# Kernel tuning notes

Hardware: AMD Instinct MI355X
Metric: run time of the kernel (lower is better)

## Reference

```python
import jax, jax.numpy as jnp
import numpy as np

T, B, D, H = 64, 512, 768, 12
HD = D // H
EPS = 1e-8  # torch cosine_similarity eps


def setup_inputs() -> dict:
    key = jax.random.key(0)
    k0, k1, k2, k3 = jax.random.split(key, 4)
    node_embs = jax.random.normal(k0, (T, B, D), dtype=jnp.float32)
    in_proj_w = jax.random.normal(k1, (3 * D, D), dtype=jnp.float32) * 0.02
    in_proj_b = jnp.zeros((3 * D,), dtype=jnp.float32)
    out_proj_w = jax.random.normal(k2, (D, D), dtype=jnp.float32) * 0.02
    out_proj_b = jnp.zeros((D,), dtype=jnp.float32)
    return {"node_embs": node_embs, "in_proj_w": in_proj_w, "in_proj_b": in_proj_b,
            "out_proj_w": out_proj_w, "out_proj_b": out_proj_b}


def reference(node_embs, in_proj_w, in_proj_b, out_proj_w, out_proj_b):
    # node_embs: (T, B, D). Original loops over t calling MHA on (B, 1, D)
    # i.e. self-attention across the B axis with batch=1, fused here over T.
    qkv = jnp.einsum('tbd,ed->tbe', node_embs, in_proj_w) + in_proj_b  # (T, B, 3D)
    q, k, v = jnp.split(qkv, 3, axis=-1)

    def heads(x):  # (T, B, D) -> (T, H, B, HD)
        return x.reshape(T, B, H, HD).transpose(0, 2, 1, 3)

    q, k, v = heads(q), heads(k), heads(v)
    scores = jnp.einsum('thqd,thkd->thqk', q, k) / np.sqrt(HD).astype(np.float32)
    attn = jax.nn.softmax(scores, axis=-1)
    ctx = jnp.einsum('thqk,thkd->thqd', attn, v)  # (T, H, B, HD)
    ctx = ctx.transpose(0, 2, 1, 3).reshape(T, B, D)
    out = jnp.einsum('tbd,ed->tbe', ctx, out_proj_w) + out_proj_b  # (T, B, D)

    # cosine similarity between all pairs over B, then mean over first index
    norm = jnp.maximum(jnp.linalg.norm(out, axis=-1), EPS)  # (T, B)
    xn = out / norm[..., None]
    sim = jnp.einsum('tid,tjd->tij', xn, xn)  # (T, B, B)
    adj = sim.mean(axis=1)[..., None]  # (T, B, 1) == (T, B, N) with N=1
    return adj
```

## Files before the change

### kernel.cpp

```cpp
#include <hip/hip_runtime.h>

#define T_ 64
#define B_ 512
#define D_ 768
#define H_ 12
#define HD_ 64
#define M1 (T_*B_)
#define N_QKV (3*D_)

typedef __attribute__((ext_vector_type(8))) short short8;
typedef __attribute__((ext_vector_type(4))) float f32x4;

__device__ __forceinline__ unsigned short f2b(float f) {
  unsigned int u = __float_as_uint(f);
  u = (u + 0x7FFFu + ((u >> 16) & 1u)) >> 16;
  return (unsigned short)u;
}
__device__ __forceinline__ float b2f(unsigned short s) {
  return __uint_as_float(((unsigned int)s) << 16);
}

__device__ __forceinline__ void load_lds16(const unsigned short* g, unsigned short* l) {
  __builtin_amdgcn_global_load_lds(
      (const __attribute__((address_space(1))) unsigned int*)g,
      (__attribute__((address_space(3))) unsigned int*)l, 16, 0, 0);
}

#define N4_NODE 6291456
#define N4_WQKV 442368
#define N4_WOUT 147456
__global__ __launch_bounds__(256) void k_cast_all(
    const float* __restrict__ node, const float* __restrict__ wqkv,
    const float* __restrict__ wout, unsigned short* __restrict__ x_bf,
    unsigned short* __restrict__ wqkv_bf, unsigned short* __restrict__ wout_bf) {
  int i = blockIdx.x * 256 + threadIdx.x;
  const float* src; unsigned short* dst; int off;
  if (i < N4_NODE)                 { src = node; dst = x_bf;    off = i; }
  else if (i < N4_NODE + N4_WQKV)  { src = wqkv; dst = wqkv_bf; off = i - N4_NODE; }
  else                             { src = wout; dst = wout_bf; off = i - N4_NODE - N4_WQKV; }
  float4 v = ((const float4*)src)[off];
  ushort4 o;
  o.x = f2b(v.x); o.y = f2b(v.y); o.z = f2b(v.z); o.w = f2b(v.w);
  ((ushort4*)dst)[off] = o;
}

#define GEMM_BODY(Aptr, Bptr) \
  unsigned short* As = Sbuf; \
  unsigned short* Bs = Sbuf + 8192; \
  const int lane = tid & 63, wave = tid >> 6; \
  const int ln = lane & 15, quad = lane >> 4; \
  const int wm = (wave & 1) * 64, wn = (wave >> 1) * 64; \
  f32x4 acc[4][4] = {}; \
  for (int k0 = 0; k0 < 768; k0 += 64) { \
    __syncthreads(); \
    _Pragma("unroll") \
    for (int it = 0; it < 4; it++) { \
      int s = wave*256 + it*64 + lane; \
      int r = s >> 3, cp = s & 7, c = cp ^ (r & 7); \
      load_lds16(&Aptr[(size_t)(m0+r)*768 + k0 + c*8], &As[s*8]); \
      load_lds16(&Bptr[(size_t)(n0+r)*768 + k0 + c*8], &Bs[s*8]); \
    } \
    __syncthreads(); \
    _Pragma("unroll") \
    for (int j = 0; j < 2; j++) { \
      short8 a[4], b[4]; \
      _Pragma("unroll") \
      for (int i = 0; i < 4; i++) { \
        int row = wm + i*16 + ln; \
        int cp = (j*4 + quad) ^ (row & 7); \
        a[i] = *(const short8*)&As[row*64 + cp*8]; \
      } \
      _Pragma("unroll") \
      for (int i = 0; i < 4; i++) { \
        int row = wn + i*16 + ln; \
        int cp = (j*4 + quad) ^ (row & 7); \
        b[i] = *(const short8*)&Bs[row*64 + cp*8]; \
      } \
      _Pragma("unroll") \
      for (int mi = 0; mi < 4; mi++) \
        _Pragma("unroll") \
        for (int ni = 0; ni < 4; ni++) \
          acc[mi][ni] = __builtin_amdgcn_mfma_f32_16x16x32_bf16(a[mi], b[ni], acc[mi][ni], 0, 0, 0); \
    } \
  }

#define EPILOG_REPACK(BIASEXPR) \
  __syncthreads(); \
  _Pragma("unroll") \
  for (int ni = 0; ni < 4; ni++) { \
    int col = wn + ni*16 + ln; \
    float bi = (BIASEXPR); \
    _Pragma("unroll") \
    for (int mi = 0; mi < 4; mi++) { \
      int row = wm + mi*16 + quad*4; \
      _Pragma("unroll") \
      for (int r = 0; r < 4; r++) \
        Sbuf[(row + r)*136 + col] = f2b(acc[mi][ni][r] + bi); \
    } \
  } \
  __syncthreads();

__global__ __launch_bounds__(256) void k_gemm_qkv(
    const unsigned short* __restrict__ A,
    const unsigned short* __restrict__ Bw,
    const float* __restrict__ bias,
    unsigned short* __restrict__ qo,
    unsigned short* __restrict__ ko,
    unsigned short* __restrict__ vTo)
{
  __shared__ __align__(16) unsigned short Sbuf[128*136];
  const int tid = threadIdx.x;
  const int bb = blockIdx.x;
  const int xcd = bb & 7, idx = bb >> 3;
  const int m0 = (xcd*32 + idx/18) * 128;
  const int n0 = (idx%18) * 128;
  GEMM_BODY(A, Bw)
  const int t = m0 >> 9;

  if (n0 < 1536) {
    EPILOG_REPACK(bias[n0 + col])
    unsigned short* dst = (n0 < 768) ? qo : ko;
    const int colbase = (n0 < 768) ? n0 : (n0 - 768);
#pragma unroll
    for (int kk = 0; kk < 8; kk++) {
      int ci = kk*256 + tid;
      int r2 = ci >> 4, c2 = (ci & 15) * 8;
      int within = colbase + c2;
      int h = within >> 6, hd = within & 63;
      *(uint4*)&dst[((size_t)(t*H_ + h)*B_ + (m0 & 511) + r2)*HD_ + hd] =
          *(const uint4*)&Sbuf[r2*136 + c2];
    }
  } else {
    __syncthreads();
#pragma unroll
    for (int mi = 0; mi < 4; mi++)
#pragma unroll
      for (int ni = 0; ni < 4; ni++) {
        int col = wn + ni*16 + ln;
        int row = wm + mi*16 + quad*4;
        float bi = bias[n0 + col];
        ushort4 pk;
        pk.x = f2b(acc[mi][ni][0] + bi);
        pk.y = f2b(acc[mi][ni][1] + bi);
        pk.z = f2b(acc[mi][ni][2] + bi);
        pk.w = f2b(acc[mi][ni][3] + bi);
        *(ushort4*)&Sbuf[col*136 + row] = pk;
      }
    __syncthreads();
#pragma unroll
    for (int kk = 0; kk < 8; kk++) {
      int ci = kk*256 + tid;
      int r2 = ci >> 4, c2 = (ci & 15) * 8;
      int cg = (n0 - 1536) + r2;
      int h = cg >> 6, hd = cg & 63;
      *(uint4*)&vTo[((size_t)(t*H_ + h)*HD_ + hd)*B_ + (m0 & 511) + c2] =
          *(const uint4*)&Sbuf[r2*136 + c2];
    }
  }
}

__global__ __launch_bounds__(256) void k_gemm_out(
    const unsigned short* __restrict__ A,
    const unsigned short* __restrict__ Bw,
    const float* __restrict__ bias,
    unsigned short* __restrict__ outb)
{
  __shared__ __align__(16) unsigned short Sbuf[128*136];
  const int tid = threadIdx.x;
  const int bb = blockIdx.x;
  const int xcd = bb & 7, idx = bb >> 3;
  const int m0 = (xcd*32 + idx/6) * 128;
  const int n0 = (idx%6) * 128;
  GEMM_BODY(A, Bw)
  EPILOG_REPACK(bias[n0 + col])
#pragma unroll
  for (int kk = 0; kk < 8; kk++) {
    int ci = kk*256 + tid;
    int r2 = ci >> 4, c2 = (ci & 15) * 8;
    *(uint4*)&outb[(size_t)(m0 + r2)*768 + n0 + c2] = *(const uint4*)&Sbuf[r2*136 + c2];
  }
}

__global__ __launch_bounds__(512) void k_attn(
    const unsigned short* __restrict__ q,
    const unsigned short* __restrict__ k,
    const unsigned short* __restrict__ vT,
    unsigned short* __restrict__ ctx)
{
  __shared__ __align__(16) unsigned short Ks[64*64];
  __shared__ __align__(16) unsigned short VT[64*64];
  __shared__ __align__(16) unsigned short Ps[8*32*72];
  __shared__ float Dn[8*64];
  const int tid = threadIdx.x;
  const int lane = tid & 63, wave = tid >> 6;
  const int ln = lane & 15, quad = lane >> 4;
  const int pxr = 8 * (ln >> 2);
  const int bb = blockIdx.x;
  const int xcd = bb & 7, idx = bb >> 3;
  const int th = xcd*96 + (idx >> 1);
  const int q0 = (idx & 1) * 256;
  const int t = th / H_, h = th - t*H_;
  const size_t base  = (size_t)th * (B_*HD_);
  const size_t baseT = (size_t)th * (HD_*B_);

  short8 qf[2][2];
#pragma unroll
  for (int s = 0; s < 2; s++) {
    const unsigned short* qp = &q[base + (size_t)(q0 + wave*32 + s*16 + ln)*HD_ + quad*8];
    qf[s][0] = *(const short8*)qp;
    qf[s][1] = *(const short8*)(qp + 32);
  }
  f32x4 acc[2][4] = {};
  float dpart[2] = {0.f, 0.f};
  unsigned short* Pw = &Ps[wave*32*72];

  for (int kt = 0; kt < B_; kt += 64) {
    __syncthreads();
    {
      int s = tid;
      int r = s >> 3, cp = s & 7, c = cp ^ (r & 7);
      load_lds16(&k[base + (size_t)(kt + r)*HD_ + c*8], &Ks[s*8]);
      load_lds16(&vT[baseT + (size_t)r*B_ + kt + c*8], &VT[s*8]);
    }
    __syncthreads();
    f32x4 sf[2][4] = {};
#pragma unroll
    for (int ki = 0; ki < 4; ki++) {
      int row = ki*16 + ln;
      short8 kf0 = *(const short8*)&Ks[row*64 + (quad     ^ (row & 7))*8];
      short8 kf1 = *(const short8*)&Ks[row*64 + ((4+quad) ^ (row & 7))*8];
#pragma unroll
      for (int s = 0; s < 2; s++) {
        sf[s][ki] = __builtin_amdgcn_mfma_f32_16x16x32_bf16(kf0, qf[s][0], sf[s][ki], 0, 0, 0);
        sf[s][ki] = __builtin_amdgcn_mfma_f32_16x16x32_bf16(kf1, qf[s][1], sf[s][ki], 0, 0, 0);
      }
    }
#pragma unroll
    for (int s = 0; s < 2; s++)
#pragma unroll
      for (int ki = 0; ki < 4; ki++) {
        float p0 = __expf(sf[s][ki][0] * 0.125f);
        float p1 = __expf(sf[s][ki][1] * 0.125f);
        float p2 = __expf(sf[s][ki][2] * 0.125f);
        float p3 = __expf(sf[s][ki][3] * 0.125f);
        dpart[s] += (p0 + p1) + (p2 + p3);
        uint2 uu;
        uu.x = (__float_as_uint(p1) & 0xFFFF0000u) | (__float_as_uint(p0) >> 16);
        uu.y = (__float_as_uint(p3) & 0xFFFF0000u) | (__float_as_uint(p2) >> 16);
        int col = (ki*16 + quad*4) ^ pxr;
        *(uint2*)&Pw[(s*16 + ln)*72 + col] = uu;
      }
    short8 pa[2][2];
#pragma unroll
    for (int s = 0; s < 2; s++)
#pragma unroll
      for (int hf = 0; hf < 2; hf++)
        pa[s][hf] = *(const short8*)&Pw[(s*16 + ln)*72 + ((hf*32 + quad*8) ^ pxr)];
#pragma unroll
    for (int ds = 0; ds < 4; ds++) {
      int row = ds*16 + ln;
      short8 vb0 = *(const short8*)&VT[row*64 + (quad     ^ (row & 7))*8];
      short8 vb1 = *(const short8*)&VT[row*64 + ((4+quad) ^ (row & 7))*8];
#pragma unroll
      for (int s = 0; s < 2; s++) {
        acc[s][ds] = __builtin_amdgcn_mfma_f32_16x16x32_bf16(pa[s][0], vb0, acc[s][ds], 0, 0, 0);
        acc[s][ds] = __builtin_amdgcn_mfma_f32_16x16x32_bf16(pa[s][1], vb1, acc[s][ds], 0, 0, 0);
      }
    }
  }
#pragma unroll
  for (int s = 0; s < 2; s++) {
    float d = dpart[s];
    d += __shfl_xor(d, 16);
    d += __shfl_xor(d, 32);
    if (quad == 0) Dn[wave*64 + s*16 + ln] = d;
  }
#pragma unroll
  for (int s = 0; s < 2; s++) {
    int qrow = q0 + wave*32 + s*16 + quad*4;
#pragma unroll
    for (int r = 0; r < 4; r++) {
      float invd = 1.f / Dn[wave*64 + s*16 + quad*4 + r];
      size_t o = ((size_t)t*B_ + (qrow + r))*D_ + h*HD_ + ln;
#pragma unroll
      for (int ds = 0; ds < 4; ds++)
        ctx[o + ds*16] = f2b(acc[s][ds][r] * invd);
    }
  }
}

__global__ __launch_bounds__(256) void k_norms1(const unsigned short* __restrict__ outb,
                                                float* __restrict__ norms,
                                                float* __restrict__ pmvec)
{
  __shared__ float wsum[4*768];
  int blk = blockIdx.x;
  int t = blk >> 3, c = blk & 7;
  int wave = threadIdx.x >> 6, lane = threadIdx.x & 63;
  float macc[12];
#pragma unroll
  for (int j = 0; j < 12; j++) macc[j] = 0.f;
  for (int i = 0; i < 16; i++) {
    int b = c*64 + wave*16 + i;
    const unsigned short* row = &outb[((size_t)t*B_ + b)*D_];
    float x[12]; float ss = 0.f;
#pragma unroll
    for (int j = 0; j < 12; j++) { x[j] = b2f(row[lane + 64*j]); ss += x[j]*x[j]; }
#pragma unroll
    for (int off = 32; off; off >>= 1) ss += __shfl_xor(ss, off);
    float nr = fmaxf(sqrtf(ss), 1e-8f);
    if (lane == 0) norms[(size_t)t*B_ + b] = nr;
    float inv = 1.f / nr;
#pragma unroll
    for (int j = 0; j < 12; j++) macc[j] += x[j]*inv;
  }
#pragma unroll
  for (int j = 0; j < 12; j++) wsum[wave*768 + 64*j + lane] = macc[j];
  __syncthreads();
  for (int d = threadIdx.x; d < 768; d += 256) {
    pmvec[(size_t)blk*768 + d] = wsum[d] + wsum[768 + d] + wsum[1536 + d] + wsum[2304 + d];
  }
}

__global__ __launch_bounds__(256) void k_norms2(const float* __restrict__ pmvec,
                                                float* __restrict__ mvec)
{
  int t = blockIdx.x;
  for (int d = threadIdx.x; d < 768; d += 256) {
    float s = 0.f;
#pragma unroll
    for (int c = 0; c < 8; c++) s += pmvec[(size_t)(t*8 + c)*768 + d];
    mvec[t*768 + d] = s * (1.0f/512.0f);
  }
}

__global__ __launch_bounds__(256) void k_adj(const unsigned short* __restrict__ outb,
                                             const float* __restrict__ norms,
                                             const float* __restrict__ mvec,
                                             float* __restrict__ adj)
{
  int idx = blockIdx.x*4 + (threadIdx.x >> 6);
  int lane = threadIdx.x & 63;
  int t = idx >> 9;
  const unsigned short* row = &outb[(size_t)idx*768];
  const float* m = &mvec[t*768];
  float dot = 0.f;
#pragma unroll
  for (int j = 0; j < 12; j++) dot += b2f(row[lane + 64*j]) * m[lane + 64*j];
#pragma unroll
  for (int off = 32; off; off >>= 1) dot += __shfl_xor(dot, off);
  if (lane == 0) adj[idx] = dot / norms[idx];
}

extern "C" void kernel_launch(void* const* d_in, const int* in_sizes, int n_in,
                              void* d_out, int out_size, void* d_ws, size_t ws_size,
                              hipStream_t stream)
{
  const float* node = (const float*)d_in[0];
  const float* wqkv = (const float*)d_in[1];
  const float* bqkv = (const float*)d_in[2];
  const float* wout = (const float*)d_in[3];
  const float* bout = (const float*)d_in[4];
  float* adj = (float*)d_out;

  char* ws = (char*)d_ws;
  const size_t SZ = (size_t)M1*D_*2;
  unsigned short* q_bf    = (unsigned short*)(ws);
  unsigned short* k_bf    = (unsigned short*)(ws + SZ);
  unsigned short* vT_bf   = (unsigned short*)(ws + 2*SZ);
  unsigned short* ctx_bf  = (unsigned short*)(ws + 3*SZ);
  unsigned short* x_bf    = (unsigned short*)(ws + 4*SZ);
  unsigned short* wqkv_bf = (unsigned short*)(ws + 5*SZ);
  unsigned short* wout_bf = (unsigned short*)(ws + 5*SZ + 3538944);
  unsigned short* out_bf  = (unsigned short*)(ws);
  float* pmvec            = (float*)(ws + 4*SZ);
  float* norms            = (float*)(ws + 5*SZ + 3538944 + 1179648);
  float* mvec             = (float*)(ws + 5*SZ + 3538944 + 1179648 + 131072);

  k_cast_all<<<26880, 256, 0, stream>>>(node, wqkv, wout, x_bf, wqkv_bf, wout_bf);
  k_gemm_qkv<<<4608, 256, 0, stream>>>(x_bf, wqkv_bf, bqkv, q_bf, k_bf, vT_bf);
  k_attn<<<1536, 512, 0, stream>>>(q_bf, k_bf, vT_bf, ctx_bf);
  k_gemm_out<<<1536, 256, 0, stream>>>(ctx_bf, wout_bf, bout, out_bf);
  k_norms1<<<T_*8, 256, 0, stream>>>(out_bf, norms, pmvec);
  k_norms2<<<T_, 256, 0, stream>>>(pmvec, mvec);
  k_adj<<<M1/4, 256, 0, stream>>>(out_bf, norms, mvec, adj);
}
```

Measured before the change: 445.3 us.

## Rewrite projection GEMMs as 256x256 tiles with 8-wave double-buffered pipelined K-loop

Replaces the 128x128 GEMM tiles in the QKV and output projections with 256x256 tiles computed by 512-thread blocks. The K-loop double-buffers 128KB of dynamic LDS and interleaves async global-to-LDS loads with MFMA quadrants, using explicit waitcnt, barriers and s_setprio. The goal is to raise arithmetic intensity and hide global-load latency behind matrix work. In exchange the LDS footprint is much larger, there are fewer blocks (384 for the output GEMM) and the hand-tuned ordering of barriers and waits is fragile.

```diff
diff --git a/kernel.cpp b/kernel.cpp
--- a/kernel.cpp
+++ b/kernel.cpp
@@ -44,63 +44,111 @@
   ((ushort4*)dst)[off] = o;
 }
 
-#define GEMM_BODY(Aptr, Bptr) \
-  unsigned short* As = Sbuf; \
-  unsigned short* Bs = Sbuf + 8192; \
+#define BAR() __builtin_amdgcn_s_barrier()
+#define WAIT_LGKM0() asm volatile("s_waitcnt lgkmcnt(0)" ::: "memory")
+#define WAIT_VM8() asm volatile("s_waitcnt vmcnt(8)" ::: "memory")
+#define WAIT_VM6() asm volatile("s_waitcnt vmcnt(6)" ::: "memory")
+#define WAIT_VM0() asm volatile("s_waitcnt vmcnt(0)" ::: "memory")
+
+#define STG_A(tile, h) do { \
+  const unsigned short* g_ = Ab + (size_t)(tile)*64 + (size_t)(h)*98304; \
+  unsigned short* l_ = &lds[((tile)&1)*32768 + (h)*8192 + tid*8]; \
+  load_lds16(g_, l_); \
+  load_lds16(g_ + 49152, l_ + 4096); \
+} while (0)
+
+#define STG_B(tile, h) do { \
+  const unsigned short* g_ = Bb + (size_t)(tile)*64 + (size_t)(h)*98304; \
+  unsigned short* l_ = &lds[((tile)&1)*32768 + 16384 + (h)*8192 + tid*8]; \
+  load_lds16(g_, l_); \
+  load_lds16(g_ + 49152, l_ + 4096); \
+} while (0)
+
+#define RD_A(tile, mh) do { \
+  _Pragma("unroll") \
+  for (int mf = 0; mf < 4; mf++) { \
+    const int rh = wm*64 + mf*16 + ln; \
+    const unsigned short* p_ = &lds[((tile)&1)*32768 + (mh)*8192 + rh*64]; \
+    aF[mh][mf][0] = *(const short8*)(p_ + ((quad     ^ (rh&7))<<3)); \
+    aF[mh][mf][1] = *(const short8*)(p_ + (((4+quad) ^ (rh&7))<<3)); \
+  } \
+} while (0)
+
+#define RD_B(tile, nh) do { \
+  _Pragma("unroll") \
+  for (int nf = 0; nf < 2; nf++) { \
+    const int rh = wn*32 + nf*16 + ln; \
+    const unsigned short* p_ = &lds[((tile)&1)*32768 + 16384 + (nh)*8192 + rh*64]; \
+    bF[nh][nf][0] = *(const short8*)(p_ + ((quad     ^ (rh&7))<<3)); \
+    bF[nh][nf][1] = *(const short8*)(p_ + (((4+quad) ^ (rh&7))<<3)); \
+  } \
+} while (0)
+
+#define MM(mh, nh) do { \
+  __builtin_amdgcn_s_setprio(1); \
+  _Pragma("unroll") \
+  for (int mf = 0; mf < 4; mf++) \
+    _Pragma("unroll") \
+    for (int nf = 0; nf < 2; nf++) { \
+      acc[mh][nh][mf][nf] = __builtin_amdgcn_mfma_f32_16x16x32_bf16(aF[mh][mf][0], bF[nh][nf][0], acc[mh][nh][mf][nf], 0, 0, 0); \
+      acc[mh][nh][mf][nf] = __builtin_amdgcn_mfma_f32_16x16x32_bf16(aF[mh][mf][1], bF[nh][nf][1], acc[mh][nh][mf][nf], 0, 0, 0); \
+    } \
+  __builtin_amdgcn_s_setprio(0); \
+} while (0)
+
+#define GEMM8_KLOOP(Aptr, Bptr) \
+  const int tid = threadIdx.x; \
   const int lane = tid & 63, wave = tid >> 6; \
   const int ln = lane & 15, quad = lane >> 4; \
-  const int wm = (wave & 1) * 64, wn = (wave >> 1) * 64; \
-  f32x4 acc[4][4] = {}; \
-  for (int k0 = 0; k0 < 768; k0 += 64) { \
-    __syncthreads(); \
-    _Pragma("unroll") \
-    for (int it = 0; it < 4; it++) { \
-      int s = wave*256 + it*64 + lane; \
-      int r = s >> 3, cp = s & 7, c = cp ^ (r & 7); \
-      load_lds16(&Aptr[(size_t)(m0+r)*768 + k0 + c*8], &As[s*8]); \
-      load_lds16(&Bptr[(size_t)(n0+r)*768 + k0 + c*8], &Bs[s*8]); \
-    } \
-    __syncthreads(); \
-    _Pragma("unroll") \
-    for (int j = 0; j < 2; j++) { \
-      short8 a[4], b[4]; \
-      _Pragma("unroll") \
-      for (int i = 0; i < 4; i++) { \
-        int row = wm + i*16 + ln; \
-        int cp = (j*4 + quad) ^ (row & 7); \
-        a[i] = *(const short8*)&As[row*64 + cp*8]; \
-      } \
-      _Pragma("unroll") \
-      for (int i = 0; i < 4; i++) { \
-        int row = wn + i*16 + ln; \
-        int cp = (j*4 + quad) ^ (row & 7); \
-        b[i] = *(const short8*)&Bs[row*64 + cp*8]; \
-      } \
-      _Pragma("unroll") \
-      for (int mi = 0; mi < 4; mi++) \
-        _Pragma("unroll") \
-        for (int ni = 0; ni < 4; ni++) \
-          acc[mi][ni] = __builtin_amdgcn_mfma_f32_16x16x32_bf16(a[mi], b[ni], acc[mi][ni], 0, 0, 0); \
-    } \
-  }
-
-#define EPILOG_REPACK(BIASEXPR) \
-  __syncthreads(); \
-  _Pragma("unroll") \
-  for (int ni = 0; ni < 4; ni++) { \
-    int col = wn + ni*16 + ln; \
-    float bi = (BIASEXPR); \
-    _Pragma("unroll") \
-    for (int mi = 0; mi < 4; mi++) { \
-      int row = wm + mi*16 + quad*4; \
-      _Pragma("unroll") \
-      for (int r = 0; r < 4; r++) \
-        Sbuf[(row + r)*136 + col] = f2b(acc[mi][ni][r] + bi); \
-    } \
+  const int wm = wave & 1, wn = wave >> 1; \
+  const int r0 = tid >> 3, c0 = (tid & 7) ^ (r0 & 7); \
+  const unsigned short* Ab = Aptr + (size_t)(m0 + r0)*768 + c0*8; \
+  const unsigned short* Bb = Bptr + (size_t)(n0 + r0)*768 + c0*8; \
+  short8 aF[2][4][2]; \
+  short8 bF[2][2][2]; \
+  f32x4 acc[2][2][4][2] = {}; \
+   \
+  STG_A(0,0); STG_B(0,0); STG_B(0,1); STG_A(0,1); \
+  STG_A(1,0); STG_B(1,0); STG_B(1,1); STG_A(1,1); \
+  WAIT_VM8(); BAR(); \
+  RD_A(0,0); RD_B(0,0); \
+  WAIT_LGKM0(); BAR(); \
+  STG_A(2,0); \
+  for (int J = 0; J < 5; ++J) { \
+    const int cur = 2*J, nxt = 2*J+1, nn = 2*J+2, nn1 = 2*J+3, nn2 = 2*J+4; \
+     WAIT_VM6(); \
+    RD_B(cur,1); STG_B(nn,0); \
+    BAR(); WAIT_LGKM0(); MM(0,0); BAR(); \
+     RD_A(cur,1); STG_B(nn,1); \
+    BAR(); WAIT_LGKM0(); MM(0,1); BAR(); \
+     RD_A(nxt,0); STG_A(nn,1); \
+    BAR(); WAIT_LGKM0(); MM(1,0); BAR(); \
+     RD_B(nxt,0); STG_A(nn1,0); \
+    BAR(); WAIT_LGKM0(); MM(1,1); BAR(); \
+     WAIT_VM6(); \
+    RD_B(nxt,1); STG_B(nn1,0); \
+    BAR(); WAIT_LGKM0(); MM(0,0); BAR(); \
+     RD_A(nxt,1); STG_B(nn1,1); \
+    BAR(); WAIT_LGKM0(); MM(0,1); BAR(); \
+     RD_A(nn,0); STG_A(nn1,1); \
+    BAR(); WAIT_LGKM0(); MM(1,0); BAR(); \
+     RD_B(nn,0); \
+    if (J < 4) { STG_A(nn2,0); } \
+    BAR(); WAIT_LGKM0(); MM(1,1); BAR(); \
   } \
+   \
+  WAIT_VM0(); \
+  RD_B(10,1); BAR(); WAIT_LGKM0(); MM(0,0); BAR(); \
+  RD_A(10,1); BAR(); WAIT_LGKM0(); MM(0,1); BAR(); \
+  RD_A(11,0); BAR(); WAIT_LGKM0(); MM(1,0); BAR(); \
+  RD_B(11,0); BAR(); WAIT_LGKM0(); MM(1,1); BAR(); \
+  RD_B(11,1); BAR(); WAIT_LGKM0(); MM(0,0); BAR(); \
+  RD_A(11,1); BAR(); WAIT_LGKM0(); MM(0,1); BAR(); \
+  MM(1,0); \
+  MM(1,1); \
   __syncthreads();
 
-__global__ __launch_bounds__(256) void k_gemm_qkv(
+__global__ __launch_bounds__(512, 2) void k_gemm_qkv8(
     const unsigned short* __restrict__ A,
     const unsigned short* __restrict__ Bw,
     const float* __restrict__ bias,
@@ -108,76 +156,118 @@
     unsigned short* __restrict__ ko,
     unsigned short* __restrict__ vTo)
 {
-  __shared__ __align__(16) unsigned short Sbuf[128*136];
-  const int tid = threadIdx.x;
+  extern __shared__ __align__(16) unsigned short lds[];
   const int bb = blockIdx.x;
   const int xcd = bb & 7, idx = bb >> 3;
-  const int m0 = (xcd*32 + idx/18) * 128;
-  const int n0 = (idx%18) * 128;
-  GEMM_BODY(A, Bw)
-  const int t = m0 >> 9;
-
+  const int m0 = (xcd*16 + idx/9) * 256;
+  const int n0 = (idx%9) * 256;
+  GEMM8_KLOOP(A, Bw)
+
+  const int t = m0 >> 9, mb = m0 & 511;
   if (n0 < 1536) {
-    EPILOG_REPACK(bias[n0 + col])
+#pragma unroll
+    for (int mh = 0; mh < 2; mh++)
+#pragma unroll
+    for (int nh = 0; nh < 2; nh++)
+#pragma unroll
+    for (int nf = 0; nf < 2; nf++) {
+      const int col = nh*128 + wn*32 + nf*16 + ln;
+      const float bi = bias[n0 + col];
+      const int cc = col >> 3, cs = col & 7;
+#pragma unroll
+      for (int mf = 0; mf < 4; mf++) {
+        const int row = mh*128 + wm*64 + mf*16 + quad*4;
+#pragma unroll
+        for (int r = 0; r < 4; r++) {
+          const int rw = row + r;
+          lds[rw*256 + ((cc ^ (rw&7))<<3) + cs] = f2b(acc[mh][nh][mf][nf][r] + bi);
+        }
+      }
+    }
+    __syncthreads();
     unsigned short* dst = (n0 < 768) ? qo : ko;
-    const int colbase = (n0 < 768) ? n0 : (n0 - 768);
-#pragma unroll
-    for (int kk = 0; kk < 8; kk++) {
-      int ci = kk*256 + tid;
-      int r2 = ci >> 4, c2 = (ci & 15) * 8;
-      int within = colbase + c2;
+    const int colbase = (n0 < 768) ? n0 : n0 - 768;
+#pragma unroll
+    for (int it = 0; it < 16; it++) {
+      int ci = it*512 + tid;
+      int r2 = ci >> 5, cj = ci & 31;
+      int within = colbase + cj*8;
       int h = within >> 6, hd = within & 63;
-      *(uint4*)&dst[((size_t)(t*H_ + h)*B_ + (m0 & 511) + r2)*HD_ + hd] =
-          *(const uint4*)&Sbuf[r2*136 + c2];
+      *(uint4*)&dst[((size_t)(t*H_ + h)*B_ + mb + r2)*HD_ + hd] =
+          *(const uint4*)&lds[r2*256 + ((cj ^ (r2&7))<<3)];
     }
   } else {
+#pragma unroll
+    for (int mh = 0; mh < 2; mh++)
+#pragma unroll
+    for (int nh = 0; nh < 2; nh++)
+#pragma unroll
+    for (int nf = 0; nf < 2; nf++) {
+      const int col = nh*128 + wn*32 + nf*16 + ln;
+      const float bi = bias[n0 + col];
+#pragma unroll
+      for (int mf = 0; mf < 4; mf++) {
+        const int row = mh*128 + wm*64 + mf*16 + quad*4;
+        ushort4 pk;
+        pk.x = f2b(acc[mh][nh][mf][nf][0] + bi);
+        pk.y = f2b(acc[mh][nh][mf][nf][1] + bi);
+        pk.z = f2b(acc[mh][nh][mf][nf][2] + bi);
+        pk.w = f2b(acc[mh][nh][mf][nf][3] + bi);
+        *(ushort4*)&lds[col*256 + (((row>>3) ^ (col&7))<<3) + (row&7)] = pk;
+      }
+    }
     __syncthreads();
 #pragma unroll
-    for (int mi = 0; mi < 4; mi++)
-#pragma unroll
-      for (int ni = 0; ni < 4; ni++) {
-        int col = wn + ni*16 + ln;
-        int row = wm + mi*16 + quad*4;
-        float bi = bias[n0 + col];
-        ushort4 pk;
-        pk.x = f2b(acc[mi][ni][0] + bi);
-        pk.y = f2b(acc[mi][ni][1] + bi);
-        pk.z = f2b(acc[mi][ni][2] + bi);
-        pk.w = f2b(acc[mi][ni][3] + bi);
-        *(ushort4*)&Sbuf[col*136 + row] = pk;
-      }
-    __syncthreads();
-#pragma unroll
-    for (int kk = 0; kk < 8; kk++) {
-      int ci = kk*256 + tid;
-      int r2 = ci >> 4, c2 = (ci & 15) * 8;
+    for (int it = 0; it < 16; it++) {
+      int ci = it*512 + tid;
+      int r2 = ci >> 5, cj = ci & 31;
       int cg = (n0 - 1536) + r2;
       int h = cg >> 6, hd = cg & 63;
-      *(uint4*)&vTo[((size_t)(t*H_ + h)*HD_ + hd)*B_ + (m0 & 511) + c2] =
-          *(const uint4*)&Sbuf[r2*136 + c2];
-    }
-  }
-}
-
-__global__ __launch_bounds__(256) void k_gemm_out(
+      *(uint4*)&vTo[((size_t)(t*H_ + h)*HD_ + hd)*B_ + mb + cj*8] =
+          *(const uint4*)&lds[r2*256 + ((cj ^ (r2&7))<<3)];
+    }
+  }
+}
+
+__global__ __launch_bounds__(512, 2) void k_gemm_out8(
     const unsigned short* __restrict__ A,
     const unsigned short* __restrict__ Bw,
     const float* __restrict__ bias,
     unsigned short* __restrict__ outb)
 {
-  __shared__ __align__(16) unsigned short Sbuf[128*136];
-  const int tid = threadIdx.x;
+  extern __shared__ __align__(16) unsigned short lds[];
   const int bb = blockIdx.x;
   const int xcd = bb & 7, idx = bb >> 3;
-  const int m0 = (xcd*32 + idx/6) * 128;
-  const int n0 = (idx%6) * 128;
-  GEMM_BODY(A, Bw)
-  EPILOG_REPACK(bias[n0 + col])
-#pragma unroll
-  for (int kk = 0; kk < 8; kk++) {
-    int ci = kk*256 + tid;
-    int r2 = ci >> 4, c2 = (ci & 15) * 8;
-    *(uint4*)&outb[(size_t)(m0 + r2)*768 + n0 + c2] = *(const uint4*)&Sbuf[r2*136 + c2];
+  const int m0 = (xcd*16 + idx/3) * 256;
+  const int n0 = (idx%3) * 256;
+  GEMM8_KLOOP(A, Bw)
+
+#pragma unroll
+  for (int mh = 0; mh < 2; mh++)
+#pragma unroll
+  for (int nh = 0; nh < 2; nh++)
+#pragma unroll
+  for (int nf = 0; nf < 2; nf++) {
+    const int col = nh*128 + wn*32 + nf*16 + ln;
+    const float bi = bias[n0 + col];
+    const int cc = col >> 3, cs = col & 7;
+#pragma unroll
+    for (int mf = 0; mf < 4; mf++) {
+      const int row = mh*128 + wm*64 + mf*16 + quad*4;
+#pragma unroll
+      for (int r = 0; r < 4; r++) {
+        const int rw = row + r;
+        lds[rw*256 + ((cc ^ (rw&7))<<3) + cs] = f2b(acc[mh][nh][mf][nf][r] + bi);
+      }
+    }
+  }
+  __syncthreads();
+#pragma unroll
+  for (int it = 0; it < 16; it++) {
+    int ci = it*512 + tid;
+    int r2 = ci >> 5, cj = ci & 31;
+    *(uint4*)&outb[(size_t)(m0 + r2)*768 + n0 + cj*8] =
+        *(const uint4*)&lds[r2*256 + ((cj ^ (r2&7))<<3)];
   }
 }
 
@@ -377,10 +467,19 @@
   float* norms            = (float*)(ws + 5*SZ + 3538944 + 1179648);
   float* mvec             = (float*)(ws + 5*SZ + 3538944 + 1179648 + 131072);
 
+  static int shmem_set = 0;
+  if (!shmem_set) {
+    hipFuncSetAttribute((const void*)k_gemm_qkv8,
+                        hipFuncAttributeMaxDynamicSharedMemorySize, 131072);
+    hipFuncSetAttribute((const void*)k_gemm_out8,
+                        hipFuncAttributeMaxDynamicSharedMemorySize, 131072);
+    shmem_set = 1;
+  }
+
   k_cast_all<<<26880, 256, 0, stream>>>(node, wqkv, wout, x_bf, wqkv_bf, wout_bf);
-  k_gemm_qkv<<<4608, 256, 0, stream>>>(x_bf, wqkv_bf, bqkv, q_bf, k_bf, vT_bf);
+  k_gemm_qkv8<<<1152, 512, 131072, stream>>>(x_bf, wqkv_bf, bqkv, q_bf, k_bf, vT_bf);
   k_attn<<<1536, 512, 0, stream>>>(q_bf, k_bf, vT_bf, ctx_bf);
-  k_gemm_out<<<1536, 256, 0, stream>>>(ctx_bf, wout_bf, bout, out_bf);
+  k_gemm_out8<<<384, 512, 131072, stream>>>(ctx_bf, wout_bf, bout, out_bf);
   k_norms1<<<T_*8, 256, 0, stream>>>(out_bf, norms, pmvec);
   k_norms2<<<T_, 256, 0, stream>>>(pmvec, mvec);
   k_adj<<<M1/4, 256, 0, stream>>>(out_bf, norms, mvec, adj);
```

After: 661.0 us. 48.4% more time.
